# Kernel tuning notes

Measured on AMD Instinct MI355X. Metric: run time of the kernel, lower is better.

The kernel has to match this reference:

```python
import jax, jax.numpy as jnp
import numpy as np

N, M, D, DV = 8192, 8192, 64, 64

def setup_inputs() -> dict:
    key = jax.random.key(0)
    kq, kk, kv = jax.random.split(key, 3)
    Q = jax.random.normal(kq, (N, D), dtype=jnp.float32)
    K = jax.random.normal(kk, (M, D), dtype=jnp.float32)
    V = jax.random.normal(kv, (M, DV), dtype=jnp.float32)
    return {"Q": Q, "K": K, "V": V}

def reference(Q, K, V):
    d = K.shape[-1]
    scores = jnp.einsum('nd,md->nm', Q, K) / jnp.sqrt(jnp.float32(d))  # [N, M]
    attn = jax.nn.softmax(scores, axis=-1)
    return attn @ V  # [N, DV]
```

## Files before the change

kernel.cpp:

```cpp
#include <hip/hip_runtime.h>


#define NQ 8192
#define NK 8192

typedef float f32x4 __attribute__((ext_vector_type(4)));
typedef short short8 __attribute__((ext_vector_type(8)));
union U4 { uint4 u; short8 s; };

#define MFMA16 __builtin_amdgcn_mfma_f32_16x16x32_bf16

__device__ __forceinline__ unsigned pk2(float a, float b) {
    unsigned ua = __builtin_bit_cast(unsigned, a);
    unsigned ub = __builtin_bit_cast(unsigned, b);
    ua = (ua + 0x7FFFu + ((ua >> 16) & 1u)) >> 16;
    ub = (ub + 0x7FFFu + ((ub >> 16) & 1u)) & 0xFFFF0000u;
    return ua | ub;
}

__device__ __forceinline__ unsigned pkt(float a, float b) {
    return __builtin_amdgcn_perm(__builtin_bit_cast(unsigned, b),
                                 __builtin_bit_cast(unsigned, a), 0x07060302u);
}

__global__ __launch_bounds__(256)
void prepass(const float* __restrict__ Kg, const float* __restrict__ Vg,
             uint4* __restrict__ Kb4, uint4* __restrict__ Vt4) {
    __shared__ float ld[64 * 33];
    const int t = threadIdx.x, b = blockIdx.x;

    if (b < 256) {
        const int kl = t >> 3, dg = t & 7;
        const int e = kl & 1, i16 = kl >> 1, h = dg >> 2, q = dg & 3;
        const float* gp = Kg + (size_t)(b * 32 + kl) * 64 + dg * 8;
        float4 f0 = *(const float4*)gp;
        float4 f1 = *(const float4*)(gp + 4);
        uint4 o = make_uint4(pk2(f0.x, f0.y), pk2(f0.z, f0.w),
                             pk2(f1.x, f1.y), pk2(f1.z, f1.w));
        Kb4[(size_t)(b * 4 + e * 2 + h) * 64 + i16 * 4 + q] = o;
    } else {
        const int c = b - 256;
        {
            const int key = t >> 3, dg = t & 7;
            const float* gp = Vg + (size_t)(c * 32 + key) * 64 + dg * 8;
            float4 f0 = *(const float4*)gp;
            float4 f1 = *(const float4*)(gp + 4);
            ld[(dg * 8 + 0) * 33 + key] = f0.x;
            ld[(dg * 8 + 1) * 33 + key] = f0.y;
            ld[(dg * 8 + 2) * 33 + key] = f0.z;
            ld[(dg * 8 + 3) * 33 + key] = f0.w;
            ld[(dg * 8 + 4) * 33 + key] = f1.x;
            ld[(dg * 8 + 5) * 33 + key] = f1.y;
            ld[(dg * 8 + 6) * 33 + key] = f1.z;
            ld[(dg * 8 + 7) * 33 + key] = f1.w;
        }
        __syncthreads();
        {
            const int dim = t >> 2, kq = t & 3;
            const int dt = dim >> 4, i16 = dim & 15;
            float v[8];
            #pragma unroll
            for (int j = 0; j < 8; ++j) v[j] = ld[dim * 33 + kq * 8 + j];
            uint4 o = make_uint4(pk2(v[0], v[1]), pk2(v[2], v[3]),
                                 pk2(v[4], v[5]), pk2(v[6], v[7]));
            Vt4[(size_t)(c * 4 + dt) * 64 + i16 * 4 + kq] = o;
        }
    }
}

__global__ __launch_bounds__(512, 1)
void attn_main(const float* __restrict__ Qg,
               const uint4* __restrict__ Kb4,
               const uint4* __restrict__ Vt4,
               float* __restrict__ Opart,
               float* __restrict__ Lpart) {
    __shared__ uint4 shb4[4160];
    float* sF = (float*)shb4;
    unsigned* shu = (unsigned*)shb4;

    const int t = threadIdx.x, w = t >> 6, lane = t & 63;
    const int q = lane >> 4, i16 = lane & 15;
    const int rw = w >> 2;
    const int kc = w & 3;
    const int bid = blockIdx.x;
    const int kh = bid & 1;
    const int rg = bid >> 1;
    const int qb0 = rg * 64;
    const int lsl = i16 * 4 + q;
    const int phase = rg & 31;

    const float SCL = 0.18033688011112042f;
    short8 aq[2][2];
    #pragma unroll
    for (int rt = 0; rt < 2; ++rt) {
        const float* qp = Qg + (size_t)(qb0 + rw * 32 + rt * 16 + i16) * 64 + q * 8;
        float4 f0 = *(const float4*)(qp);
        float4 f1 = *(const float4*)(qp + 4);
        U4 u;
        u.u = make_uint4(pk2(f0.x * SCL, f0.y * SCL), pk2(f0.z * SCL, f0.w * SCL),
                         pk2(f1.x * SCL, f1.y * SCL), pk2(f1.z * SCL, f1.w * SCL));
        aq[rt][0] = u.s;
        f0 = *(const float4*)(qp + 32);
        f1 = *(const float4*)(qp + 36);
        u.u = make_uint4(pk2(f0.x * SCL, f0.y * SCL), pk2(f0.z * SCL, f0.w * SCL),
                         pk2(f1.x * SCL, f1.y * SCL), pk2(f1.z * SCL, f1.w * SCL));
        aq[rt][1] = u.s;
    }

    f32x4 acc[2][4];
    float lsum[2][4];
    #pragma unroll
    for (int rt = 0; rt < 2; ++rt) {
        #pragma unroll
        for (int dt = 0; dt < 4; ++dt) { acc[rt][dt][0]=0.f; acc[rt][dt][1]=0.f; acc[rt][dt][2]=0.f; acc[rt][dt][3]=0.f; }
        #pragma unroll
        for (int r = 0; r < 4; ++r) lsum[rt][r] = 0.f;
    }

    const int tpw = ((i16 >> 2) & 1) + 2 * q + 32 * (i16 >> 3);
    const int pp  = i16 & 3;
    const int tpr = (q & 1) + 2 * ((i16 >> 2) & 3) + 8 * (i16 & 3) + 32 * (q >> 1);

    uint4 kfA[4], vfA[4], kfB[4], vfB[4], kfC[4], vfC[4];

#define LOAD_T(TT, KD, VD)                                                           \
    do {                                                                             \
        const int cb = ((kh << 7) + ((((TT) + phase) & 31) * 4 + kc)) * 4;           \
        _Pragma("unroll")                                                            \
        for (int eh = 0; eh < 4; ++eh)                                               \
            (KD)[eh] = Kb4[(size_t)(cb + eh) * 64 + lsl];                            \
        _Pragma("unroll")                                                            \
        for (int dt = 0; dt < 4; ++dt)                                               \
            (VD)[dt] = Vt4[(size_t)(cb + dt) * 64 + lsl];                            \
    } while (0)

#define QKEXP(KD, PAR)                                                               \
    do {                                                                             \
        _Pragma("unroll")                                                            \
        for (int rt = 0; rt < 2; ++rt) {                                             \
            f32x4 s0, s1;                                                            \
            s0[0]=-16.f; s0[1]=-16.f; s0[2]=-16.f; s0[3]=-16.f;                      \
            s1[0]=-16.f; s1[1]=-16.f; s1[2]=-16.f; s1[3]=-16.f;                      \
            U4 u0, u1, u2, u3;                                                       \
            u0.u = (KD)[0]; u1.u = (KD)[1]; u2.u = (KD)[2]; u3.u = (KD)[3];          \
            s0 = MFMA16(aq[rt][0], u0.s, s0, 0, 0, 0);                               \
            s0 = MFMA16(aq[rt][1], u1.s, s0, 0, 0, 0);                               \
            s1 = MFMA16(aq[rt][0], u2.s, s1, 0, 0, 0);                               \
            s1 = MFMA16(aq[rt][1], u3.s, s1, 0, 0, 0);                               \
            const int rbase = (((w * 2 + rt) * 2) + (PAR)) * 256;                    \
            _Pragma("unroll")                                                        \
            for (int r = 0; r < 4; ++r) {                                            \
                float p0 = __builtin_amdgcn_exp2f(s0[r]);                            \
                float p1 = __builtin_amdgcn_exp2f(s1[r]);                            \
                lsum[rt][r] += p0;                                                   \
                lsum[rt][r] += p1;                                                   \
                shu[rbase + (tpw + 8 * r) * 4 + pp] = pkt(p0, p1);                   \
            }                                                                        \
        }                                                                            \
    } while (0)

#define PVS(VD, PAR)                                                                 \
    do {                                                                             \
        U4 ap[2];                                                                    \
        _Pragma("unroll")                                                            \
        for (int rt = 0; rt < 2; ++rt)                                               \
            ap[rt].u = shb4[(((w * 2 + rt) * 2) + (PAR)) * 64 + tpr];                \
        _Pragma("unroll")                                                            \
        for (int dt = 0; dt < 4; ++dt) {                                             \
            U4 bv; bv.u = (VD)[dt];                                                  \
            _Pragma("unroll")                                                        \
            for (int rt = 0; rt < 2; ++rt)                                           \
                acc[rt][dt] = MFMA16(ap[rt].s, bv.s, acc[rt][dt], 0, 0, 0);          \
        }                                                                            \
    } while (0)

    LOAD_T(0, kfA, vfA);
    LOAD_T(1, kfB, vfB);
    LOAD_T(2, kfC, vfC);
    __builtin_amdgcn_sched_barrier(0);
    QKEXP(kfA, 0);
    #pragma unroll 1
    for (int tt = 1; tt < 31; tt += 6) {
        QKEXP(kfB, 1); PVS(vfA, 0); LOAD_T(tt + 2, kfA, vfA);
        __builtin_amdgcn_sched_barrier(0);
        QKEXP(kfC, 0); PVS(vfB, 1); LOAD_T(tt + 3, kfB, vfB);
        __builtin_amdgcn_sched_barrier(0);
        QKEXP(kfA, 1); PVS(vfC, 0); LOAD_T(tt + 4, kfC, vfC);
        __builtin_amdgcn_sched_barrier(0);
        QKEXP(kfB, 0); PVS(vfA, 1); LOAD_T(tt + 5, kfA, vfA);
        __builtin_amdgcn_sched_barrier(0);
        QKEXP(kfC, 1); PVS(vfB, 0); LOAD_T(tt + 6, kfB, vfB);
        __builtin_amdgcn_sched_barrier(0);
        QKEXP(kfA, 0); PVS(vfC, 1); LOAD_T(tt + 7, kfC, vfC);
        __builtin_amdgcn_sched_barrier(0);
    }
    QKEXP(kfB, 1);
    PVS(vfA, 0);
    PVS(vfB, 1);

    #pragma unroll
    for (int rt = 0; rt < 2; ++rt)
        #pragma unroll
        for (int r = 0; r < 4; ++r) {
            float v = lsum[rt][r];
            v += __shfl_xor(v, 1);
            v += __shfl_xor(v, 2);
            v += __shfl_xor(v, 4);
            v += __shfl_xor(v, 8);
            lsum[rt][r] = v;
        }

    __syncthreads();
    for (int step = 2; step >= 1; step >>= 1) {
        if (kc >= step && kc < 2 * step) {
            float* base = sF + (w - step) * 2080;
            #pragma unroll
            for (int rt = 0; rt < 2; ++rt) {
                #pragma unroll
                for (int dt = 0; dt < 4; ++dt)
                    #pragma unroll
                    for (int r = 0; r < 4; ++r)
                        base[(rt * 16 + 4 * q + r) * 64 + dt * 16 + i16] = acc[rt][dt][r];
                if (i16 == 0) {
                    #pragma unroll
                    for (int r = 0; r < 4; ++r) base[2048 + rt * 16 + 4 * q + r] = lsum[rt][r];
                }
            }
        }
        __syncthreads();
        if (kc < step) {
            const float* base = sF + w * 2080;
            #pragma unroll
            for (int rt = 0; rt < 2; ++rt) {
                #pragma unroll
                for (int dt = 0; dt < 4; ++dt)
                    #pragma unroll
                    for (int r = 0; r < 4; ++r)
                        acc[rt][dt][r] += base[(rt * 16 + 4 * q + r) * 64 + dt * 16 + i16];
                #pragma unroll
                for (int r = 0; r < 4; ++r) lsum[rt][r] += base[2048 + rt * 16 + 4 * q + r];
            }
        }
        __syncthreads();
    }

    if (kc == 0) {
        #pragma unroll
        for (int rt = 0; rt < 2; ++rt) {
            #pragma unroll
            for (int dt = 0; dt < 4; ++dt)
                #pragma unroll
                for (int r = 0; r < 4; ++r) {
                    const int row = qb0 + rw * 32 + rt * 16 + 4 * q + r;
                    Opart[((size_t)kh * 8192 + row) * 64 + dt * 16 + i16] = acc[rt][dt][r];
                }
            if (i16 == 0) {
                #pragma unroll
                for (int r = 0; r < 4; ++r)
                    Lpart[kh * 8192 + qb0 + rw * 32 + rt * 16 + 4 * q + r] = lsum[rt][r];
            }
        }
    }
}

__global__ __launch_bounds__(256)
void merge(const float* __restrict__ Opart, const float* __restrict__ Lpart,
           float* __restrict__ Og) {
    const int idx = blockIdx.x * 256 + threadIdx.x;
    const int row = idx >> 4, seg = idx & 15;
    const float4 a = *(const float4*)(Opart + (size_t)row * 64 + seg * 4);
    const float4 b = *(const float4*)(Opart + ((size_t)8192 + row) * 64 + seg * 4);
    const float inv = 1.0f / (Lpart[row] + Lpart[8192 + row]);
    float4 o;
    o.x = (a.x + b.x) * inv;
    o.y = (a.y + b.y) * inv;
    o.z = (a.z + b.z) * inv;
    o.w = (a.w + b.w) * inv;
    *(float4*)(Og + (size_t)row * 64 + seg * 4) = o;
}

extern "C" void kernel_launch(void* const* d_in, const int* in_sizes, int n_in,
                              void* d_out, int out_size, void* d_ws, size_t ws_size,
                              hipStream_t stream) {
    const float* Q = (const float*)d_in[0];
    const float* K = (const float*)d_in[1];
    const float* V = (const float*)d_in[2];
    float* O = (float*)d_out;
    char* ws = (char*)d_ws;
    uint4* Kb4   = (uint4*)ws;
    uint4* Vt4   = (uint4*)(ws + (1 << 20));
    float* Opart = (float*)(ws + (2 << 20));
    float* Lpart = (float*)(ws + (6 << 20));
    hipLaunchKernelGGL(prepass, dim3(512), dim3(256), 0, stream, K, V, Kb4, Vt4);
    hipLaunchKernelGGL(attn_main, dim3(256), dim3(512), 0, stream, Q, Kb4, Vt4, Opart, Lpart);
    hipLaunchKernelGGL(merge, dim3(512), dim3(256), 0, stream, Opart, Lpart, O);
}
```

Before: 99.21 us.

## Stage K tiles into LDS via async global_load_lds with 1024-thread blocks

Doubles the block to 16 waves, each handling 8 key chunks per tile instead of 4, with 16 tile iterations. K tiles are now double-buffered in LDS through asynchronous global-to-LDS loads shared by the waves, while V stays in registers loaded per tile. The register triple-buffered software pipeline is replaced by a block-wide __syncthreads per step, and the cross-wave reduction grows to three levels. The aim is to cut per-wave global K traffic and register pressure and raise latency hiding. In exchange it adds barrier stalls and more LDS use.

```diff
diff --git a/kernel.cpp b/kernel.cpp
--- a/kernel.cpp
+++ b/kernel.cpp
@@ -21,6 +21,12 @@
 __device__ __forceinline__ unsigned pkt(float a, float b) {
     return __builtin_amdgcn_perm(__builtin_bit_cast(unsigned, b),
                                  __builtin_bit_cast(unsigned, a), 0x07060302u);
+}
+
+__device__ __forceinline__ void async16(const uint4* g, uint4* l) {
+    __builtin_amdgcn_global_load_lds(
+        (const __attribute__((address_space(1))) void*)g,
+        (__attribute__((address_space(3))) void*)l, 16, 0, 0);
 }
 
 __global__ __launch_bounds__(256)
@@ -68,32 +74,32 @@
     }
 }
 
-__global__ __launch_bounds__(512, 1)
+__global__ __launch_bounds__(1024)
 void attn_main(const float* __restrict__ Qg,
                const uint4* __restrict__ Kb4,
                const uint4* __restrict__ Vt4,
                float* __restrict__ Opart,
                float* __restrict__ Lpart) {
-    __shared__ uint4 shb4[4160];
+    __shared__ uint4 shb4[8192];
     float* sF = (float*)shb4;
     unsigned* shu = (unsigned*)shb4;
 
     const int t = threadIdx.x, w = t >> 6, lane = t & 63;
     const int q = lane >> 4, i16 = lane & 15;
-    const int rw = w >> 2;
-    const int kc = w & 3;
+    const int rh = w >> 3;
+    const int kc = w & 7;
     const int bid = blockIdx.x;
     const int kh = bid & 1;
     const int rg = bid >> 1;
     const int qb0 = rg * 64;
     const int lsl = i16 * 4 + q;
-    const int phase = rg & 31;
+    const int phase = rg & 15;
 
     const float SCL = 0.18033688011112042f;
     short8 aq[2][2];
     #pragma unroll
     for (int rt = 0; rt < 2; ++rt) {
-        const float* qp = Qg + (size_t)(qb0 + rw * 32 + rt * 16 + i16) * 64 + q * 8;
+        const float* qp = Qg + (size_t)(qb0 + rh * 32 + rt * 16 + i16) * 64 + q * 8;
         float4 f0 = *(const float4*)(qp);
         float4 f1 = *(const float4*)(qp + 4);
         U4 u;
@@ -121,82 +127,94 @@
     const int pp  = i16 & 3;
     const int tpr = (q & 1) + 2 * ((i16 >> 2) & 3) + 8 * (i16 & 3) + 32 * (q >> 1);
 
-    uint4 kfA[4], vfA[4], kfB[4], vfB[4], kfC[4], vfC[4];
-
-#define LOAD_T(TT, KD, VD)                                                           \
-    do {                                                                             \
-        const int cb = ((kh << 7) + ((((TT) + phase) & 31) * 4 + kc)) * 4;           \
-        _Pragma("unroll")                                                            \
-        for (int eh = 0; eh < 4; ++eh)                                               \
-            (KD)[eh] = Kb4[(size_t)(cb + eh) * 64 + lsl];                            \
-        _Pragma("unroll")                                                            \
-        for (int dt = 0; dt < 4; ++dt)                                               \
-            (VD)[dt] = Vt4[(size_t)(cb + dt) * 64 + lsl];                            \
+    uint4 vf[4];
+
+#define DMA_K(TT, B)                                                          \
+    do {                                                                      \
+        const int Tp = ((TT) + phase) & 15;                                   \
+        _Pragma("unroll")                                                     \
+        for (int i = 0; i < 2; ++i) {                                         \
+            const int o = w * 128 + i * 64;                                   \
+            const int cg = (kh << 7) + Tp * 8 + (o >> 8);                     \
+            async16(Kb4 + (size_t)(cg * 4 + ((o >> 6) & 3)) * 64 + lane,      \
+                    shb4 + (B) * 2048 + o);                                   \
+        }                                                                     \
     } while (0)
 
-#define QKEXP(KD, PAR)                                                               \
-    do {                                                                             \
-        _Pragma("unroll")                                                            \
-        for (int rt = 0; rt < 2; ++rt) {                                             \
-            f32x4 s0, s1;                                                            \
-            s0[0]=-16.f; s0[1]=-16.f; s0[2]=-16.f; s0[3]=-16.f;                      \
-            s1[0]=-16.f; s1[1]=-16.f; s1[2]=-16.f; s1[3]=-16.f;                      \
-            U4 u0, u1, u2, u3;                                                       \
-            u0.u = (KD)[0]; u1.u = (KD)[1]; u2.u = (KD)[2]; u3.u = (KD)[3];          \
-            s0 = MFMA16(aq[rt][0], u0.s, s0, 0, 0, 0);                               \
-            s0 = MFMA16(aq[rt][1], u1.s, s0, 0, 0, 0);                               \
-            s1 = MFMA16(aq[rt][0], u2.s, s1, 0, 0, 0);                               \
-            s1 = MFMA16(aq[rt][1], u3.s, s1, 0, 0, 0);                               \
-            const int rbase = (((w * 2 + rt) * 2) + (PAR)) * 256;                    \
-            _Pragma("unroll")                                                        \
-            for (int r = 0; r < 4; ++r) {                                            \
-                float p0 = __builtin_amdgcn_exp2f(s0[r]);                            \
-                float p1 = __builtin_amdgcn_exp2f(s1[r]);                            \
-                lsum[rt][r] += p0;                                                   \
-                lsum[rt][r] += p1;                                                   \
-                shu[rbase + (tpw + 8 * r) * 4 + pp] = pkt(p0, p1);                   \
-            }                                                                        \
-        }                                                                            \
+#define LOADV(TT)                                                             \
+    do {                                                                      \
+        const int Tp = ((TT) + phase) & 15;                                   \
+        const int cg = (kh << 7) + Tp * 8 + kc;                               \
+        _Pragma("unroll")                                                     \
+        for (int dt = 0; dt < 4; ++dt)                                        \
+            vf[dt] = Vt4[(size_t)(cg * 4 + dt) * 64 + lsl];                   \
     } while (0)
 
-#define PVS(VD, PAR)                                                                 \
-    do {                                                                             \
-        U4 ap[2];                                                                    \
-        _Pragma("unroll")                                                            \
-        for (int rt = 0; rt < 2; ++rt)                                               \
-            ap[rt].u = shb4[(((w * 2 + rt) * 2) + (PAR)) * 64 + tpr];                \
-        _Pragma("unroll")                                                            \
-        for (int dt = 0; dt < 4; ++dt) {                                             \
-            U4 bv; bv.u = (VD)[dt];                                                  \
-            _Pragma("unroll")                                                        \
-            for (int rt = 0; rt < 2; ++rt)                                           \
-                acc[rt][dt] = MFMA16(ap[rt].s, bv.s, acc[rt][dt], 0, 0, 0);          \
-        }                                                                            \
+#define QKEXP(B, PAR)                                                         \
+    do {                                                                      \
+        const uint4* kbuf = shb4 + (B) * 2048 + kc * 256;                     \
+        U4 u0, u1, u2, u3;                                                    \
+        u0.u = kbuf[0 * 64 + lsl];                                            \
+        u1.u = kbuf[1 * 64 + lsl];                                            \
+        u2.u = kbuf[2 * 64 + lsl];                                            \
+        u3.u = kbuf[3 * 64 + lsl];                                            \
+        _Pragma("unroll")                                                     \
+        for (int rt = 0; rt < 2; ++rt) {                                      \
+            f32x4 s0, s1;                                                     \
+            s0[0]=-16.f; s0[1]=-16.f; s0[2]=-16.f; s0[3]=-16.f;               \
+            s1[0]=-16.f; s1[1]=-16.f; s1[2]=-16.f; s1[3]=-16.f;               \
+            s0 = MFMA16(aq[rt][0], u0.s, s0, 0, 0, 0);                        \
+            s0 = MFMA16(aq[rt][1], u1.s, s0, 0, 0, 0);                        \
+            s1 = MFMA16(aq[rt][0], u2.s, s1, 0, 0, 0);                        \
+            s1 = MFMA16(aq[rt][1], u3.s, s1, 0, 0, 0);                        \
+            const int rbase = (4096 + (((w * 2 + rt) * 2) + (PAR)) * 64) * 4; \
+            _Pragma("unroll")                                                 \
+            for (int r = 0; r < 4; ++r) {                                     \
+                float p0 = __builtin_amdgcn_exp2f(s0[r]);                     \
+                float p1 = __builtin_amdgcn_exp2f(s1[r]);                     \
+                lsum[rt][r] += p0;                                            \
+                lsum[rt][r] += p1;                                            \
+                shu[rbase + (tpw + 8 * r) * 4 + pp] = pkt(p0, p1);            \
+            }                                                                 \
+        }                                                                     \
     } while (0)
 
-    LOAD_T(0, kfA, vfA);
-    LOAD_T(1, kfB, vfB);
-    LOAD_T(2, kfC, vfC);
-    __builtin_amdgcn_sched_barrier(0);
-    QKEXP(kfA, 0);
+#define PVS(PAR)                                                              \
+    do {                                                                      \
+        U4 ap0, ap1;                                                          \
+        ap0.u = shb4[4096 + (((w * 2 + 0) * 2) + (PAR)) * 64 + tpr];          \
+        ap1.u = shb4[4096 + (((w * 2 + 1) * 2) + (PAR)) * 64 + tpr];          \
+        _Pragma("unroll")                                                     \
+        for (int dt = 0; dt < 4; ++dt) {                                      \
+            U4 bv; bv.u = vf[dt];                                             \
+            acc[0][dt] = MFMA16(ap0.s, bv.s, acc[0][dt], 0, 0, 0);            \
+            acc[1][dt] = MFMA16(ap1.s, bv.s, acc[1][dt], 0, 0, 0);            \
+        }                                                                     \
+    } while (0)
+
+    DMA_K(0, 0);
+    __syncthreads();
+    DMA_K(1, 1);
+    QKEXP(0, 0);
+    LOADV(0);
+    __syncthreads();
     #pragma unroll 1
-    for (int tt = 1; tt < 31; tt += 6) {
-        QKEXP(kfB, 1); PVS(vfA, 0); LOAD_T(tt + 2, kfA, vfA);
-        __builtin_amdgcn_sched_barrier(0);
-        QKEXP(kfC, 0); PVS(vfB, 1); LOAD_T(tt + 3, kfB, vfB);
-        __builtin_amdgcn_sched_barrier(0);
-        QKEXP(kfA, 1); PVS(vfC, 0); LOAD_T(tt + 4, kfC, vfC);
-        __builtin_amdgcn_sched_barrier(0);
-        QKEXP(kfB, 0); PVS(vfA, 1); LOAD_T(tt + 5, kfA, vfA);
-        __builtin_amdgcn_sched_barrier(0);
-        QKEXP(kfC, 1); PVS(vfB, 0); LOAD_T(tt + 6, kfB, vfB);
-        __builtin_amdgcn_sched_barrier(0);
-        QKEXP(kfA, 0); PVS(vfC, 1); LOAD_T(tt + 7, kfC, vfC);
-        __builtin_amdgcn_sched_barrier(0);
-    }
-    QKEXP(kfB, 1);
-    PVS(vfA, 0);
-    PVS(vfB, 1);
+    for (int tt = 1; tt < 15; tt += 2) {
+        DMA_K(tt + 1, 0);
+        QKEXP(1, 1);
+        PVS(0);
+        LOADV(tt);
+        __syncthreads();
+        DMA_K(tt + 2, 1);
+        QKEXP(0, 0);
+        PVS(1);
+        LOADV(tt + 1);
+        __syncthreads();
+    }
+    QKEXP(1, 1);
+    PVS(0);
+    LOADV(15);
+    PVS(1);
 
     #pragma unroll
     for (int rt = 0; rt < 2; ++rt)
@@ -211,9 +229,10 @@
         }
 
     __syncthreads();
-    for (int step = 2; step >= 1; step >>= 1) {
+    #pragma unroll 1
+    for (int step = 4; step >= 1; step >>= 1) {
         if (kc >= step && kc < 2 * step) {
-            float* base = sF + (w - step) * 2080;
+            float* base = sF + (rh * 4 + (kc - step)) * 2080;
             #pragma unroll
             for (int rt = 0; rt < 2; ++rt) {
                 #pragma unroll
@@ -229,7 +248,7 @@
         }
         __syncthreads();
         if (kc < step) {
-            const float* base = sF + w * 2080;
+            const float* base = sF + (rh * 4 + kc) * 2080;
             #pragma unroll
             for (int rt = 0; rt < 2; ++rt) {
                 #pragma unroll
@@ -251,13 +270,13 @@
             for (int dt = 0; dt < 4; ++dt)
                 #pragma unroll
                 for (int r = 0; r < 4; ++r) {
-                    const int row = qb0 + rw * 32 + rt * 16 + 4 * q + r;
+                    const int row = qb0 + rh * 32 + rt * 16 + 4 * q + r;
                     Opart[((size_t)kh * 8192 + row) * 64 + dt * 16 + i16] = acc[rt][dt][r];
                 }
             if (i16 == 0) {
                 #pragma unroll
                 for (int r = 0; r < 4; ++r)
-                    Lpart[kh * 8192 + qb0 + rw * 32 + rt * 16 + 4 * q + r] = lsum[rt][r];
+                    Lpart[kh * 8192 + qb0 + rh * 32 + rt * 16 + 4 * q + r] = lsum[rt][r];
             }
         }
     }
@@ -292,6 +311,6 @@
     float* Opart = (float*)(ws + (2 << 20));
     float* Lpart = (float*)(ws + (6 << 20));
     hipLaunchKernelGGL(prepass, dim3(512), dim3(256), 0, stream, K, V, Kb4, Vt4);
-    hipLaunchKernelGGL(attn_main, dim3(256), dim3(512), 0, stream, Q, Kb4, Vt4, Opart, Lpart);
+    hipLaunchKernelGGL(attn_main, dim3(256), dim3(1024), 0, stream, Q, Kb4, Vt4, Opart, Lpart);
     hipLaunchKernelGGL(merge, dim3(512), dim3(256), 0, stream, Opart, Lpart, O);
 }
```

Result: no change. 101.1 us (+1.9%).
